# Performance work log

Measured on AMD Instinct MI355X. Metric: run time of the kernel, lower is better.

## Reference

```python
import jax, jax.numpy as jnp
import numpy as np

SIZE = 4096
N_ITER = 10
TEMP = 0.1


def setup_inputs() -> dict:
    key = jax.random.key(0)
    kx, kw = jax.random.split(key)
    x = jax.random.normal(kx, (4, 2048, SIZE), dtype=jnp.float32)
    weight = jax.random.normal(kw, (SIZE, SIZE), dtype=jnp.float32)
    r_prev = jnp.zeros((SIZE, 1), dtype=jnp.float32)
    c_prev = jnp.zeros((1, SIZE), dtype=jnp.float32)
    return {"x": x, "weight": weight, "r_prev": r_prev, "c_prev": c_prev}


def reference(x, weight, r_prev, c_prev):
    Q = weight / TEMP  # [S, S]

    def body(i, rc):
        r, c = rc
        r = -jax.nn.logsumexp(Q + c, axis=1, keepdims=True)  # [S, 1]
        c = -jax.nn.logsumexp(Q + r, axis=0, keepdims=True)  # [1, S]
        return (r, c)

    r, c = jax.lax.fori_loop(0, N_ITER, body, (r_prev, c_prev))
    P = jnp.exp(Q + r + c)  # doubly-stochastic-ish [S, S]
    # F.linear(x, P) == x @ P.T
    return jnp.einsum('btd,od->bto', x, P)
```

## Files before the change

### kernel.cpp

```cpp
#include <hip/hip_runtime.h>


#define L2E 1.44269504088896340736f

typedef __attribute__((ext_vector_type(8))) short bf16x8;
typedef __attribute__((ext_vector_type(4))) float f32x4;

__device__ __forceinline__ unsigned short f2bf(float x) {
  unsigned u = __float_as_uint(x);
  u += 0x7fffu + ((u >> 16) & 1u);
  return (unsigned short)(u >> 16);
}
__device__ __forceinline__ float bf2f(short x) {
  return __uint_as_float(((unsigned)(unsigned short)x) << 16);
}

__global__ void prep_e(const float* __restrict__ W, unsigned short* __restrict__ E,
                       float* __restrict__ v1) {
  const int row = blockIdx.x;
  const int t = threadIdx.x;
  const float* wp = W + ((size_t)row << 12);
  float v[16];
  float m = -3.4e38f;
#pragma unroll
  for (int ch = 0; ch < 4; ++ch) {
    float4 wv = *(const float4*)(wp + ch * 1024 + t * 4);
    float a0 = 10.f * wv.x, a1 = 10.f * wv.y, a2 = 10.f * wv.z, a3 = 10.f * wv.w;
    v[ch * 4 + 0] = a0; v[ch * 4 + 1] = a1; v[ch * 4 + 2] = a2; v[ch * 4 + 3] = a3;
    m = fmaxf(m, fmaxf(fmaxf(a0, a1), fmaxf(a2, a3)));
  }
#pragma unroll
  for (int off = 32; off > 0; off >>= 1) m = fmaxf(m, __shfl_xor(m, off));
  __shared__ float sm[4], ss[4];
  if ((t & 63) == 0) sm[t >> 6] = m;
  __syncthreads();
  m = fmaxf(fmaxf(sm[0], sm[1]), fmaxf(sm[2], sm[3]));
  unsigned short* ep = E + ((size_t)row << 12);
  float s = 0.f;
#pragma unroll
  for (int ch = 0; ch < 4; ++ch) {
    float e0 = exp2f((v[ch * 4 + 0] - m) * L2E);
    float e1 = exp2f((v[ch * 4 + 1] - m) * L2E);
    float e2 = exp2f((v[ch * 4 + 2] - m) * L2E);
    float e3 = exp2f((v[ch * 4 + 3] - m) * L2E);
    s += (e0 + e1) + (e2 + e3);
    ushort4 o;
    o.x = f2bf(e0); o.y = f2bf(e1); o.z = f2bf(e2); o.w = f2bf(e3);
    *(ushort4*)(ep + ch * 1024 + t * 4) = o;
  }
#pragma unroll
  for (int off = 32; off > 0; off >>= 1) s += __shfl_xor(s, off);
  if ((t & 63) == 0) ss[t >> 6] = s;
  __syncthreads();
  if (t == 0) v1[row] = 1.f / ((ss[0] + ss[1]) + (ss[2] + ss[3]));
}

__global__ void transpose_bf(const unsigned short* __restrict__ E,
                             unsigned short* __restrict__ ET) {
  __shared__ unsigned short tile[64][66];
  const int t = threadIdx.x;
  const int r = t >> 3;
  const int c8 = (t & 7) << 3;
  const size_t i0 = (size_t)blockIdx.y << 6;
  const size_t j0 = (size_t)blockIdx.x << 6;
#pragma unroll
  for (int h = 0; h < 2; ++h) {
    bf16x8 vv = *(const bf16x8*)(E + (i0 + h * 32 + r) * 4096 + j0 + c8);
#pragma unroll
    for (int e = 0; e < 8; ++e) tile[h * 32 + r][c8 + e] = (unsigned short)vv[e];
  }
  __syncthreads();
#pragma unroll
  for (int h = 0; h < 2; ++h) {
    bf16x8 vv;
#pragma unroll
    for (int e = 0; e < 8; ++e) vv[e] = (short)tile[c8 + e][h * 32 + r];
    *(bf16x8*)(ET + (j0 + h * 32 + r) * 4096 + i0 + c8) = vv;
  }
}

__global__ void recip_mv(const unsigned short* __restrict__ M,
                         const float* __restrict__ uin, float* __restrict__ vout) {
  const int t = threadIdx.x;
  const int l = t & 63, w = t >> 6;
  const int row = (blockIdx.x << 2) + w;
  const unsigned short* mp = M + ((size_t)row << 12);
  float s = 0.f;
#pragma unroll
  for (int ch = 0; ch < 8; ++ch) {
    const int j = (ch << 9) + (l << 3);
    bf16x8 e = *(const bf16x8*)(mp + j);
    const float4 u0 = *(const float4*)(uin + j);
    const float4 u1 = *(const float4*)(uin + j + 4);
    s = fmaf(bf2f(e[0]), u0.x, s);
    s = fmaf(bf2f(e[1]), u0.y, s);
    s = fmaf(bf2f(e[2]), u0.z, s);
    s = fmaf(bf2f(e[3]), u0.w, s);
    s = fmaf(bf2f(e[4]), u1.x, s);
    s = fmaf(bf2f(e[5]), u1.y, s);
    s = fmaf(bf2f(e[6]), u1.z, s);
    s = fmaf(bf2f(e[7]), u1.w, s);
  }
#pragma unroll
  for (int off = 32; off > 0; off >>= 1) s += __shfl_xor(s, off);
  if (l == 0) vout[row] = 1.f / s;
}

__global__ void scale_x(const float* __restrict__ X, const float* __restrict__ u,
                        unsigned short* __restrict__ Y) {
  const size_t idx = ((size_t)blockIdx.x * 256 + threadIdx.x) * 4;
  const int col = (int)(idx & 4095);
  float4 xv = *(const float4*)(X + idx);
  float4 uu = *(const float4*)(u + col);
  ushort4 o;
  o.x = f2bf(xv.x * uu.x);
  o.y = f2bf(xv.y * uu.y);
  o.z = f2bf(xv.z * uu.z);
  o.w = f2bf(xv.w * uu.w);
  *(ushort4*)(Y + idx) = o;
}

__global__ __launch_bounds__(512, 2) void gemm_bt(const unsigned short* __restrict__ A,
                                                  const unsigned short* __restrict__ B,
                                                  const float* __restrict__ vscale,
                                                  float* __restrict__ C) {
  __shared__ unsigned short lds[65536];
  const int t = threadIdx.x;
  const int l = t & 63;
  const int w = t >> 6;
  const int wm = w >> 2, wn = w & 3;

  int pid = blockIdx.x;
  pid = (pid & 7) * 64 + (pid >> 3);
  const int grp = pid >> 6;
  const int rem = pid & 63;
  const int bm = (grp << 2) + (rem & 3);
  const int bn = rem >> 2;
  const int m0 = bm << 8;
  const int n0 = bn << 8;

  const int ca = (((t & 3) ^ ((t >> 3) & 3)) << 3);
  const unsigned short* gA = A + (size_t)(m0 + (t >> 2)) * 4096 + ca;
  const unsigned short* gB = B + (size_t)(n0 + (t >> 2)) * 4096 + ca;

  const int xc = (((l >> 4) ^ ((l >> 1) & 3)) << 3);
  const int aOff = (wm * 128 + (l & 15)) * 32 + xc;
  const int bOff = (wn * 64 + (l & 15)) * 32 + xc;

  auto stage = [&](const unsigned short* gbase, int h, int isB) {
    const int slot = h & 3;
    const unsigned short* g = gbase + (size_t)h * 32;
#pragma unroll
    for (int ra = 0; ra < 2; ++ra)
      __builtin_amdgcn_global_load_lds(
          (const __attribute__((address_space(1))) void*)(g + (size_t)ra * 524288),
          (__attribute__((address_space(3))) void*)((char*)lds + isB * 65536 + slot * 16384 + ra * 8192 + w * 1024),
          16, 0, 0);
  };

  f32x4 acc[8][4] = {};
  bf16x8 afr[4], bfr[4];

  stage(gA, 0, 0); stage(gB, 0, 1);
  stage(gA, 1, 0); stage(gB, 1, 1);
  asm volatile("s_waitcnt vmcnt(4)" ::: "memory");
  __builtin_amdgcn_s_barrier();

#define PHASE(SLOT, MH, STAGE_STMT, WAIT_STMT)                                     \
  {                                                                                \
    const unsigned short* aL = lds + (SLOT) * 8192 + aOff + (MH) * 2048;           \
    _Pragma("unroll")                                                              \
    for (int i = 0; i < 4; ++i) afr[i] = *(const bf16x8*)(aL + i * 512);           \
    if ((MH) == 0) {                                                               \
      const unsigned short* bL = lds + 32768 + (SLOT) * 8192 + bOff;               \
      _Pragma("unroll")                                                            \
      for (int j = 0; j < 4; ++j) bfr[j] = *(const bf16x8*)(bL + j * 512);         \
    }                                                                              \
    STAGE_STMT;                                                                    \
    __builtin_amdgcn_s_barrier();                                                  \
    asm volatile("s_waitcnt lgkmcnt(0)" ::: "memory");                             \
    __builtin_amdgcn_sched_barrier(0);                                             \
    __builtin_amdgcn_s_setprio(1);                                                 \
    _Pragma("unroll")                                                              \
    for (int i = 0; i < 4; ++i)                                                    \
      _Pragma("unroll")                                                            \
      for (int j = 0; j < 4; ++j)                                                  \
        acc[(MH) * 4 + i][j] = __builtin_amdgcn_mfma_f32_16x16x32_bf16(            \
            afr[i], bfr[j], acc[(MH) * 4 + i][j], 0, 0, 0);                        \
    __builtin_amdgcn_s_setprio(0);                                                 \
    WAIT_STMT;                                                                     \
    __builtin_amdgcn_s_barrier();                                                  \
  }

  for (int kt = 0; kt < 64; kt += 2) {
    PHASE(0, 0, { if (kt <= 62) stage(gA, 2 * kt + 2, 0); }, {})
    PHASE(0, 1, { if (kt <= 62) stage(gB, 2 * kt + 2, 1); },
          { if (kt <= 62) asm volatile("s_waitcnt vmcnt(4)" ::: "memory");
            else          asm volatile("s_waitcnt vmcnt(0)" ::: "memory"); })
    PHASE(1, 0, { if (kt <= 62) stage(gA, 2 * kt + 3, 0); }, {})
    PHASE(1, 1, { if (kt <= 62) stage(gB, 2 * kt + 3, 1); },
          { if (kt <= 62) asm volatile("s_waitcnt vmcnt(4)" ::: "memory"); })
    PHASE(2, 0, { if (kt + 1 <= 62) stage(gA, 2 * kt + 4, 0); }, {})
    PHASE(2, 1, { if (kt + 1 <= 62) stage(gB, 2 * kt + 4, 1); },
          { if (kt + 1 <= 62) asm volatile("s_waitcnt vmcnt(4)" ::: "memory");
            else              asm volatile("s_waitcnt vmcnt(0)" ::: "memory"); })
    PHASE(3, 0, { if (kt + 1 <= 62) stage(gA, 2 * kt + 5, 0); }, {})
    PHASE(3, 1, { if (kt + 1 <= 62) stage(gB, 2 * kt + 5, 1); },
          { if (kt + 1 <= 62) asm volatile("s_waitcnt vmcnt(4)" ::: "memory"); })
  }
#undef PHASE

  const int crow = (l >> 4) << 2;
  const int ccol = l & 15;
#pragma unroll
  for (int j = 0; j < 4; ++j) {
    const int colj = n0 + (wn << 6) + (j << 4) + ccol;
    const float vs = vscale[colj];
#pragma unroll
    for (int i = 0; i < 8; ++i) {
      const int rowi = m0 + (wm << 7) + (i << 4) + crow;
#pragma unroll
      for (int q = 0; q < 4; ++q)
        C[((size_t)(rowi + q) << 12) + colj] = acc[i][j][q] * vs;
    }
  }
}

extern "C" void kernel_launch(void* const* d_in, const int* in_sizes, int n_in,
                              void* d_out, int out_size, void* d_ws, size_t ws_size,
                              hipStream_t stream) {
  const float* x      = (const float*)d_in[0];
  const float* weight = (const float*)d_in[1];
  float* out = (float*)d_out;

  char* ws = (char*)d_ws;
  float* u = (float*)ws;
  float* v = (float*)(ws + (16 << 10));
  unsigned short* E  = (unsigned short*)(ws + (64 << 10));
  unsigned short* ET = E + (size_t)4096 * 4096;
  unsigned short* xb = ET;

  prep_e<<<4096, 256, 0, stream>>>(weight, E, v);
  transpose_bf<<<dim3(64, 64), 256, 0, stream>>>(E, ET);

  for (int it = 0; it < 10; ++it) {
    if (it) recip_mv<<<1024, 256, 0, stream>>>(E, u, v);
    recip_mv<<<1024, 256, 0, stream>>>(ET, v, u);
  }

  scale_x<<<32768, 256, 0, stream>>>(x, u, xb);

  gemm_bt<<<512, 512, 0, stream>>>(xb, E, v, out);
}
```

Before: 429.3 us.

## Deepen GEMM prefetch to three stages and split recip_mv accumulators

The GEMM main loop now keeps three K-tiles in flight instead of two, issuing loads for tile h+3 during phase h. The vmcnt waits are retuned to 8/4/0, and the loop is restructured into PH_A and PH_B macros. The aim is to hide global-to-LDS latency behind more MFMA work, at the cost of more outstanding loads and more intricate wait accounting. Separately, recip_mv uses four independent accumulators to break the serial FMA dependency chain.

```diff
diff --git a/kernel.cpp b/kernel.cpp
--- a/kernel.cpp
+++ b/kernel.cpp
@@ -85,22 +85,23 @@
   const int l = t & 63, w = t >> 6;
   const int row = (blockIdx.x << 2) + w;
   const unsigned short* mp = M + ((size_t)row << 12);
-  float s = 0.f;
+  float s0 = 0.f, s1 = 0.f, s2 = 0.f, s3 = 0.f;
 #pragma unroll
   for (int ch = 0; ch < 8; ++ch) {
     const int j = (ch << 9) + (l << 3);
     bf16x8 e = *(const bf16x8*)(mp + j);
     const float4 u0 = *(const float4*)(uin + j);
     const float4 u1 = *(const float4*)(uin + j + 4);
-    s = fmaf(bf2f(e[0]), u0.x, s);
-    s = fmaf(bf2f(e[1]), u0.y, s);
-    s = fmaf(bf2f(e[2]), u0.z, s);
-    s = fmaf(bf2f(e[3]), u0.w, s);
-    s = fmaf(bf2f(e[4]), u1.x, s);
-    s = fmaf(bf2f(e[5]), u1.y, s);
-    s = fmaf(bf2f(e[6]), u1.z, s);
-    s = fmaf(bf2f(e[7]), u1.w, s);
-  }
+    s0 = fmaf(bf2f(e[0]), u0.x, s0);
+    s1 = fmaf(bf2f(e[1]), u0.y, s1);
+    s2 = fmaf(bf2f(e[2]), u0.z, s2);
+    s3 = fmaf(bf2f(e[3]), u0.w, s3);
+    s0 = fmaf(bf2f(e[4]), u1.x, s0);
+    s1 = fmaf(bf2f(e[5]), u1.y, s1);
+    s2 = fmaf(bf2f(e[6]), u1.z, s2);
+    s3 = fmaf(bf2f(e[7]), u1.w, s3);
+  }
+  float s = (s0 + s1) + (s2 + s3);
 #pragma unroll
   for (int off = 32; off > 0; off >>= 1) s += __shfl_xor(s, off);
   if (l == 0) vout[row] = 1.f / s;
@@ -163,20 +164,19 @@
 
   stage(gA, 0, 0); stage(gB, 0, 1);
   stage(gA, 1, 0); stage(gB, 1, 1);
-  asm volatile("s_waitcnt vmcnt(4)" ::: "memory");
+  stage(gA, 2, 0); stage(gB, 2, 1);
+  asm volatile("s_waitcnt vmcnt(8)" ::: "memory");
   __builtin_amdgcn_s_barrier();
 
-#define PHASE(SLOT, MH, STAGE_STMT, WAIT_STMT)                                     \
+#define PH_A(HV, SLOT)                                                             \
   {                                                                                \
-    const unsigned short* aL = lds + (SLOT) * 8192 + aOff + (MH) * 2048;           \
+    const unsigned short* aL = lds + (SLOT) * 8192 + aOff;                         \
+    const unsigned short* bL = lds + 32768 + (SLOT) * 8192 + bOff;                 \
     _Pragma("unroll")                                                              \
     for (int i = 0; i < 4; ++i) afr[i] = *(const bf16x8*)(aL + i * 512);           \
-    if ((MH) == 0) {                                                               \
-      const unsigned short* bL = lds + 32768 + (SLOT) * 8192 + bOff;               \
-      _Pragma("unroll")                                                            \
-      for (int j = 0; j < 4; ++j) bfr[j] = *(const bf16x8*)(bL + j * 512);         \
-    }                                                                              \
-    STAGE_STMT;                                                                    \
+    _Pragma("unroll")                                                              \
+    for (int j = 0; j < 4; ++j) bfr[j] = *(const bf16x8*)(bL + j * 512);           \
+    if ((HV) <= 124) stage(gA, (HV) + 3, 0);                                       \
     __builtin_amdgcn_s_barrier();                                                  \
     asm volatile("s_waitcnt lgkmcnt(0)" ::: "memory");                             \
     __builtin_amdgcn_sched_barrier(0);                                             \
@@ -185,30 +185,43 @@
     for (int i = 0; i < 4; ++i)                                                    \
       _Pragma("unroll")                                                            \
       for (int j = 0; j < 4; ++j)                                                  \
-        acc[(MH) * 4 + i][j] = __builtin_amdgcn_mfma_f32_16x16x32_bf16(            \
-            afr[i], bfr[j], acc[(MH) * 4 + i][j], 0, 0, 0);                        \
+        acc[i][j] = __builtin_amdgcn_mfma_f32_16x16x32_bf16(                       \
+            afr[i], bfr[j], acc[i][j], 0, 0, 0);                                   \
     __builtin_amdgcn_s_setprio(0);                                                 \
-    WAIT_STMT;                                                                     \
-    __builtin_amdgcn_s_barrier();                                                  \
-  }
-
-  for (int kt = 0; kt < 64; kt += 2) {
-    PHASE(0, 0, { if (kt <= 62) stage(gA, 2 * kt + 2, 0); }, {})
-    PHASE(0, 1, { if (kt <= 62) stage(gB, 2 * kt + 2, 1); },
-          { if (kt <= 62) asm volatile("s_waitcnt vmcnt(4)" ::: "memory");
-            else          asm volatile("s_waitcnt vmcnt(0)" ::: "memory"); })
-    PHASE(1, 0, { if (kt <= 62) stage(gA, 2 * kt + 3, 0); }, {})
-    PHASE(1, 1, { if (kt <= 62) stage(gB, 2 * kt + 3, 1); },
-          { if (kt <= 62) asm volatile("s_waitcnt vmcnt(4)" ::: "memory"); })
-    PHASE(2, 0, { if (kt + 1 <= 62) stage(gA, 2 * kt + 4, 0); }, {})
-    PHASE(2, 1, { if (kt + 1 <= 62) stage(gB, 2 * kt + 4, 1); },
-          { if (kt + 1 <= 62) asm volatile("s_waitcnt vmcnt(4)" ::: "memory");
-            else              asm volatile("s_waitcnt vmcnt(0)" ::: "memory"); })
-    PHASE(3, 0, { if (kt + 1 <= 62) stage(gA, 2 * kt + 5, 0); }, {})
-    PHASE(3, 1, { if (kt + 1 <= 62) stage(gB, 2 * kt + 5, 1); },
-          { if (kt + 1 <= 62) asm volatile("s_waitcnt vmcnt(4)" ::: "memory"); })
-  }
-#undef PHASE
+    __builtin_amdgcn_s_barrier();                                                  \
+  }
+
+#define PH_B(HV, SLOT)                                                             \
+  {                                                                                \
+    const unsigned short* aL = lds + (SLOT) * 8192 + aOff + 2048;                  \
+    _Pragma("unroll")                                                              \
+    for (int i = 0; i < 4; ++i) afr[i] = *(const bf16x8*)(aL + i * 512);           \
+    if ((HV) <= 124) stage(gB, (HV) + 3, 1);                                       \
+    __builtin_amdgcn_s_barrier();                                                  \
+    asm volatile("s_waitcnt lgkmcnt(0)" ::: "memory");                             \
+    __builtin_amdgcn_sched_barrier(0);                                             \
+    __builtin_amdgcn_s_setprio(1);                                                 \
+    _Pragma("unroll")                                                              \
+    for (int i = 0; i < 4; ++i)                                                    \
+      _Pragma("unroll")                                                            \
+      for (int j = 0; j < 4; ++j)                                                  \
+        acc[4 + i][j] = __builtin_amdgcn_mfma_f32_16x16x32_bf16(                   \
+            afr[i], bfr[j], acc[4 + i][j], 0, 0, 0);                               \
+    __builtin_amdgcn_s_setprio(0);                                                 \
+    if ((HV) <= 124)      asm volatile("s_waitcnt vmcnt(8)" ::: "memory");         \
+    else if ((HV) == 125) asm volatile("s_waitcnt vmcnt(4)" ::: "memory");         \
+    else if ((HV) == 126) asm volatile("s_waitcnt vmcnt(0)" ::: "memory");         \
+    __builtin_amdgcn_s_barrier();                                                  \
+  }
+
+  for (int h = 0; h < 128; h += 4) {
+    PH_A(h + 0, 0) PH_B(h + 0, 0)
+    PH_A(h + 1, 1) PH_B(h + 1, 1)
+    PH_A(h + 2, 2) PH_B(h + 2, 2)
+    PH_A(h + 3, 3) PH_B(h + 3, 3)
+  }
+#undef PH_A
+#undef PH_B
 
   const int crow = (l >> 4) << 2;
   const int ccol = l & 15;
```

Result: no change. 428.0 us (median of 2 runs) (-0.3%).
